# Kernel optimization log

Hardware: AMD Instinct MI355X
Metric: run time of the kernel (lower is better)

The kernel has to match this reference:

```python
import jax, jax.numpy as jnp
import numpy as np

N = 100000   # nodes
E = 1600000  # edges
D = 128      # feature dim (layers all 128)
G = 512      # graphs in batch
C = 10       # num_classes
EPS = 1e-5   # batchnorm eps


def setup_inputs() -> dict:
    key = jax.random.key(0)
    ks = jax.random.split(key, 16)
    s = 1.0 / np.sqrt(D)
    return {
        "x": jax.random.normal(ks[0], (N, D), jnp.float32),
        "edge_index": jax.random.randint(ks[1], (2, E), 0, N),
        "batch": jnp.sort(jax.random.randint(ks[2], (N,), 0, G)),
        "w1": jax.random.normal(ks[3], (D, D), jnp.float32) * s,
        "b1": jnp.zeros((D,), jnp.float32),
        "w2": jax.random.normal(ks[4], (D, D), jnp.float32) * s,
        "b2": jnp.zeros((D,), jnp.float32),
        "w3": jax.random.normal(ks[5], (D, D), jnp.float32) * s,
        "b3": jnp.zeros((D,), jnp.float32),
        "g1": jnp.ones((D,), jnp.float32),
        "be1": jnp.zeros((D,), jnp.float32),
        "g2": jnp.ones((D,), jnp.float32),
        "be2": jnp.zeros((D,), jnp.float32),
        "fc_w": jax.random.normal(ks[6], (D, C), jnp.float32) * s,
        "fc_b": jnp.zeros((C,), jnp.float32),
    }


def _gcn(x, src, dst, norm, W, b):
    # transform -> gather -> normalize -> scatter-add (PyG GCNConv)
    h = x @ W
    out = jax.ops.segment_sum(h[src] * norm[:, None], dst, num_segments=x.shape[0])
    return out + b


def _bn(x, g, b):
    # training-mode BatchNorm1d: batch mean / biased variance
    mu = jnp.mean(x, axis=0)
    var = jnp.mean((x - mu) ** 2, axis=0)
    return (x - mu) * jax.lax.rsqrt(var + EPS) * g + b


def reference(x, edge_index, batch, w1, b1, w2, b2, w3, b3, g1, be1, g2, be2, fc_w, fc_b):
    n = x.shape[0]
    loop = jnp.arange(n)
    src = jnp.concatenate([edge_index[0], loop])  # add self-loops
    dst = jnp.concatenate([edge_index[1], loop])
    deg = jax.ops.segment_sum(jnp.ones_like(src, x.dtype), dst, num_segments=n)
    dinv = jax.lax.rsqrt(jnp.maximum(deg, 1.0))  # deg >= 1 due to self-loops
    norm = dinv[src] * dinv[dst]  # symmetric normalization per edge

    h = jax.nn.relu(_gcn(x, src, dst, norm, w1, b1))        # conv1 + relu (bn1 unused, per source)
    h = jax.nn.relu(_gcn(h, src, dst, norm, w2, b2))        # conv2 + relu
    h = jax.nn.relu(_bn(h, g1, be1))                        # bn + relu
    h = jax.nn.relu(_gcn(h, src, dst, norm, w3, b3))        # conv3 + relu
    h = jax.nn.relu(_bn(h, g2, be2))                        # bn + relu

    cnt = jax.ops.segment_sum(jnp.ones((n,), h.dtype), batch, num_segments=G)
    pooled = jax.ops.segment_sum(h, batch, num_segments=G) / jnp.maximum(cnt, 1.0)[:, None]
    logits = pooled @ fc_w + fc_b
    return jax.nn.log_softmax(logits, axis=1)
```

## Files before the change

kernel.cpp:

```cpp
#include <hip/hip_runtime.h>
#include <hip/hip_bf16.h>
#include <math.h>

#define D 128
#define G_GRAPHS 512
#define C_CLASSES 10
#define BN_EPS 1e-5f
#define NBUCK_MAX 512
#define EDGE_CHUNK 4096
#define EPT 16

typedef unsigned short u16;
typedef unsigned int u32;
typedef unsigned short ushort4_t __attribute__((ext_vector_type(4)));
typedef unsigned short ushort8_t __attribute__((ext_vector_type(8)));
typedef __bf16 bf16x8 __attribute__((ext_vector_type(8)));
typedef float floatx4 __attribute__((ext_vector_type(4)));
union B8 { ushort8_t u; bf16x8 b; };

__device__ __forceinline__ float bf_lo(u32 v) { return __uint_as_float(v << 16); }
__device__ __forceinline__ float bf_hi(u32 v) { return __uint_as_float(v & 0xffff0000u); }
__device__ __forceinline__ u16 f2bf(float f) {
    union { float f; u32 u; } x; x.f = f;
    u32 r = x.u + 0x7fff + ((x.u >> 16) & 1);
    return (u16)(r >> 16);
}
__device__ __forceinline__ u32 pack2bf(float a, float b) {
    return (u32)f2bf(a) | ((u32)f2bf(b) << 16);
}


__global__ __launch_bounds__(256) void bucket_hist_kernel(
    const int* __restrict__ dst, int* __restrict__ bucketCnt, int E, int nbuck)
{
    __shared__ int h[NBUCK_MAX];
    int tid = threadIdx.x;
    for (int i = tid; i < NBUCK_MAX; i += 256) h[i] = 0;
    __syncthreads();
    for (int i = blockIdx.x * 256 + tid; i < E; i += gridDim.x * 256)
        atomicAdd(&h[dst[i] >> 8], 1);
    __syncthreads();
    for (int i = tid; i < nbuck; i += 256)
        if (h[i]) atomicAdd(&bucketCnt[i], h[i]);
}

__global__ void scan_buckets_kernel(
    const int* __restrict__ bucketCnt, int* __restrict__ bucketBase,
    int* __restrict__ bucketCursor, int* __restrict__ rowPtr, int nbuck, int N, int E)
{
    __shared__ int buf[2][512];
    int tid = threadIdx.x;
    int v = (tid < nbuck) ? bucketCnt[tid] : 0;
    buf[0][tid] = v;
    __syncthreads();
    int cur = 0;
    for (int off = 1; off < 512; off <<= 1) {
        buf[1 - cur][tid] = buf[cur][tid] + ((tid >= off) ? buf[cur][tid - off] : 0);
        cur ^= 1;
        __syncthreads();
    }
    if (tid < nbuck) {
        int b = buf[cur][tid] - v;
        bucketBase[tid] = b;
        bucketCursor[tid] = b;
    }
    if (tid == 0) { bucketBase[nbuck] = E; rowPtr[N] = E; }
}

__global__ __launch_bounds__(256) void scatter_pairs_kernel(
    const int* __restrict__ src, const int* __restrict__ dst,
    int* __restrict__ bucketCursor, u32* __restrict__ pairs, int E)
{
    __shared__ int h[NBUCK_MAX];
    __shared__ int base[NBUCK_MAX];
    int tid = threadIdx.x;
    int e0 = blockIdx.x * EDGE_CHUNK;
    for (int i = tid; i < NBUCK_MAX; i += 256) h[i] = 0;
    __syncthreads();
    int s[EPT], d[EPT], r[EPT];
#pragma unroll
    for (int j = 0; j < EPT; ++j) {
        int i = e0 + j * 256 + tid;
        if (i < E) {
            s[j] = src[i];
            d[j] = dst[i];
            r[j] = atomicAdd(&h[d[j] >> 8], 1);
        } else {
            d[j] = -1;
        }
    }
    __syncthreads();
    for (int i = tid; i < NBUCK_MAX; i += 256)
        if (h[i]) base[i] = atomicAdd(&bucketCursor[i], h[i]);
    __syncthreads();
#pragma unroll
    for (int j = 0; j < EPT; ++j) {
        if (d[j] >= 0) {
            int b = d[j] >> 8;
            pairs[base[b] + r[j]] = ((u32)s[j] << 8) | (u32)(d[j] & 255);
        }
    }
}

__global__ __launch_bounds__(256) void bucket_sort_kernel(
    const u32* __restrict__ pairs, const int* __restrict__ bucketBase,
    int* __restrict__ colIdx, int* __restrict__ rowPtr, float* __restrict__ dinv, int N)
{
    __shared__ int h[256];
    __shared__ int cur[256];
    __shared__ int sbuf[2][256];
    int tid = threadIdx.x;
    int b = blockIdx.x;
    int s = bucketBase[b], e = bucketBase[b + 1];
    h[tid] = 0;
    __syncthreads();
    for (int i = s + tid; i < e; i += 256)
        atomicAdd(&h[pairs[i] & 255], 1);
    __syncthreads();
    int cnt = h[tid];
    sbuf[0][tid] = cnt;
    __syncthreads();
    int c = 0;
    for (int off = 1; off < 256; off <<= 1) {
        sbuf[1 - c][tid] = sbuf[c][tid] + ((tid >= off) ? sbuf[c][tid - off] : 0);
        c ^= 1;
        __syncthreads();
    }
    int excl = sbuf[c][tid] - cnt;
    int v = b * 256 + tid;
    if (v < N) {
        rowPtr[v] = s + excl;
        dinv[v] = rsqrtf((float)(cnt + 1));
    }
    cur[tid] = s + excl;
    __syncthreads();
    for (int i = s + tid; i < e; i += 256) {
        u32 p = pairs[i];
        int pos = atomicAdd(&cur[p & 255], 1);
        colIdx[pos] = (int)(p >> 8);
    }
}

__global__ __launch_bounds__(256) void graph_bounds_kernel(
    const int* __restrict__ batch, int* __restrict__ gstart, int N)
{
    int i = blockIdx.x * 256 + threadIdx.x;
    if (i >= N) return;
    int b = batch[i];
    int prev = (i == 0) ? -1 : batch[i - 1];
    if (b != prev) {
        for (int g = prev + 1; g <= b; ++g) gstart[g] = i;
    }
    if (i == N - 1) {
        for (int g = b + 1; g <= G_GRAPHS; ++g) gstart[g] = N;
    }
}

__global__ __launch_bounds__(256) void wconv_kernel(
    const float4* __restrict__ w1, const float4* __restrict__ w2,
    const float4* __restrict__ w3, u16* __restrict__ wtAll)
{
    const float4* W = (blockIdx.x == 0) ? w1 : (blockIdx.x == 1) ? w2 : w3;
    u16* Wt = wtAll + (size_t)blockIdx.x * D * D;
    int tid = threadIdx.x;
#pragma unroll
    for (int i = 0; i < 16; ++i) {
        int idx = tid + i * 256;
        int k = idx >> 5, c4 = idx & 31;
        float4 v = W[idx];
        Wt[(4 * c4 + 0) * D + k] = f2bf(v.x);
        Wt[(4 * c4 + 1) * D + k] = f2bf(v.y);
        Wt[(4 * c4 + 2) * D + k] = f2bf(v.z);
        Wt[(4 * c4 + 3) * D + k] = f2bf(v.w);
    }
}

#define XS_STRIDE 136
#define GEMM_GRID 768

__device__ __forceinline__ void gemm_core_and_store(
    const u16* Xs, const u16* Ws, u16* __restrict__ Y, int row0, int nrows, int tid)
{
    int wid = tid >> 6, lane = tid & 63;
    int m = lane & 15, quad = lane >> 4;
    int xrow = wid * 16 + m;

    floatx4 acc[8] = {};
#pragma unroll
    for (int ks = 0; ks < 4; ++ks) {
        int kk = ks * 32 + quad * 8;
        B8 a;
        a.u = *(const ushort8_t*)&Xs[xrow * XS_STRIDE + kk];
#pragma unroll
        for (int t = 0; t < 8; ++t) {
            B8 b;
            b.u = *(const ushort8_t*)&Ws[(t * 16 + m) * XS_STRIDE + kk];
            acc[t] = __builtin_amdgcn_mfma_f32_16x16x32_bf16(b.b, a.b, acc[t], 0, 0, 0);
        }
    }
    int grow = row0 + xrow;
    if (grow < nrows) {
#pragma unroll
        for (int t = 0; t < 8; ++t) {
            ushort4_t o;
            o.x = f2bf(acc[t][0]); o.y = f2bf(acc[t][1]);
            o.z = f2bf(acc[t][2]); o.w = f2bf(acc[t][3]);
            *(ushort4_t*)&Y[(size_t)grow * D + t * 16 + quad * 4] = o;
        }
    }
}

__device__ __forceinline__ void stage_w(const u16* __restrict__ Wt, u16* Ws, int tid) {
    const ushort8_t* Wv = (const ushort8_t*)Wt;
#pragma unroll
    for (int i = 0; i < 8; ++i) {
        int idx = tid + i * 256;
        int n = idx >> 4, c8 = idx & 15;
        *(ushort8_t*)&Ws[n * XS_STRIDE + c8 * 8] = Wv[idx];
    }
}

__global__ __launch_bounds__(256) void gemm_mfma_f32in_kernel(
    const float4* __restrict__ X, const u16* __restrict__ Wt,
    u16* __restrict__ Y, int nrows, int ntiles)
{
    __shared__ __align__(16) u16 Xs[64 * XS_STRIDE];
    __shared__ __align__(16) u16 Ws[128 * XS_STRIDE];
    int tid = threadIdx.x;
    stage_w(Wt, Ws, tid);
    for (int t = blockIdx.x; t < ntiles; t += gridDim.x) {
        int row0 = t * 64;
        __syncthreads();
#pragma unroll
        for (int i = 0; i < 8; ++i) {
            int idx = tid + i * 256;
            int r = idx >> 5, c4 = idx & 31;
            int gr = row0 + r;
            float4 v = make_float4(0.f, 0.f, 0.f, 0.f);
            if (gr < nrows) v = X[(size_t)gr * 32 + c4];
            ushort4_t o;
            o.x = f2bf(v.x); o.y = f2bf(v.y); o.z = f2bf(v.z); o.w = f2bf(v.w);
            *(ushort4_t*)&Xs[r * XS_STRIDE + c4 * 4] = o;
        }
        __syncthreads();
        gemm_core_and_store(Xs, Ws, Y, row0, nrows, tid);
    }
}

__global__ __launch_bounds__(256) void gemm_mfma_bf16in_kernel(
    const uint4* __restrict__ X, const u16* __restrict__ Wt,
    const float* __restrict__ gsum, const float* __restrict__ gsq,
    const float* __restrict__ gamma, const float* __restrict__ beta, float invN,
    u16* __restrict__ Y, int nrows, int ntiles)
{
    __shared__ __align__(16) u16 Xs[64 * XS_STRIDE];
    __shared__ __align__(16) u16 Ws[128 * XS_STRIDE];
    __shared__ float scs[D], shs[D];
    int tid = threadIdx.x;
    bool fuse = (gsum != nullptr);
    stage_w(Wt, Ws, tid);
    if (fuse && tid < D) {
        float mu = gsum[tid] * invN;
        float var = gsq[tid] * invN - mu * mu;
        float sc = gamma[tid] * rsqrtf(var + BN_EPS);
        scs[tid] = sc;
        shs[tid] = beta[tid] - mu * sc;
    }
    for (int t = blockIdx.x; t < ntiles; t += gridDim.x) {
        int row0 = t * 64;
        __syncthreads();
#pragma unroll
        for (int i = 0; i < 4; ++i) {
            int idx = tid + i * 256;
            int r = idx >> 4, c8 = idx & 15;
            int gr = row0 + r;
            uint4 v = make_uint4(0, 0, 0, 0);
            if (gr < nrows) v = X[(size_t)gr * 16 + c8];
            if (fuse) {
                int k = c8 * 8;
                v.x = pack2bf(fmaxf(bf_lo(v.x) * scs[k]     + shs[k],     0.f),
                              fmaxf(bf_hi(v.x) * scs[k + 1] + shs[k + 1], 0.f));
                v.y = pack2bf(fmaxf(bf_lo(v.y) * scs[k + 2] + shs[k + 2], 0.f),
                              fmaxf(bf_hi(v.y) * scs[k + 3] + shs[k + 3], 0.f));
                v.z = pack2bf(fmaxf(bf_lo(v.z) * scs[k + 4] + shs[k + 4], 0.f),
                              fmaxf(bf_hi(v.z) * scs[k + 5] + shs[k + 5], 0.f));
                v.w = pack2bf(fmaxf(bf_lo(v.w) * scs[k + 6] + shs[k + 6], 0.f),
                              fmaxf(bf_hi(v.w) * scs[k + 7] + shs[k + 7], 0.f));
            }
            *(uint4*)&Xs[r * XS_STRIDE + c8 * 8] = v;
        }
        __syncthreads();
        gemm_core_and_store(Xs, Ws, Y, row0, nrows, tid);
    }
}

#define ACC8(tw, duu)                                              \
    acc[0] += (duu) * bf_lo((tw).x); acc[1] += (duu) * bf_hi((tw).x); \
    acc[2] += (duu) * bf_lo((tw).y); acc[3] += (duu) * bf_hi((tw).y); \
    acc[4] += (duu) * bf_lo((tw).z); acc[5] += (duu) * bf_hi((tw).z); \
    acc[6] += (duu) * bf_lo((tw).w); acc[7] += (duu) * bf_hi((tw).w);

__global__ __launch_bounds__(256) void aggregate_kernel(
    const uint4* __restrict__ T, const int* __restrict__ colIdx,
    const int* __restrict__ rowPtr, const float* __restrict__ dinv,
    const float* __restrict__ bias, uint4* __restrict__ outH, int n)
{
    int wid = threadIdx.x >> 6;
    int lane = threadIdx.x & 63;
    int fg = lane & 15;
    int eg = lane >> 4;
    int row = (blockIdx.x * 4 + wid) * 4 + eg;
    bool active = row < n;

    float dr = 0.f;
    int s = 0, m = 0;
    float acc[8] = {};
    if (active) {
        dr = dinv[row];
        s = rowPtr[row];
        m = rowPtr[row + 1] - s;
        uint4 sv = T[(size_t)row * 16 + fg];
        acc[0] = dr * bf_lo(sv.x); acc[1] = dr * bf_hi(sv.x);
        acc[2] = dr * bf_lo(sv.y); acc[3] = dr * bf_hi(sv.y);
        acc[4] = dr * bf_lo(sv.z); acc[5] = dr * bf_hi(sv.z);
        acc[6] = dr * bf_lo(sv.w); acc[7] = dr * bf_hi(sv.w);
    }

    for (int c0 = 0; c0 < m; c0 += 16) {
        int mm = m - c0;
        if (mm > 16) mm = 16;
        int u = row;
        float du = 0.f;
        if (fg < mm) {
            u = colIdx[s + c0 + fg];
            du = dinv[u];
        }
        int nb = (mm + 3) >> 2;
        for (int b = 0; b < nb; ++b) {
            int base = (eg << 4) + (b << 2);
            int u0 = __shfl(u, base);     float d0 = __shfl(du, base);
            int u1 = __shfl(u, base + 1); float d1 = __shfl(du, base + 1);
            int u2 = __shfl(u, base + 2); float d2 = __shfl(du, base + 2);
            int u3 = __shfl(u, base + 3); float d3 = __shfl(du, base + 3);
            uint4 t0 = T[(size_t)u0 * 16 + fg];
            uint4 t1 = T[(size_t)u1 * 16 + fg];
            uint4 t2 = T[(size_t)u2 * 16 + fg];
            uint4 t3 = T[(size_t)u3 * 16 + fg];
            ACC8(t0, d0); ACC8(t1, d1); ACC8(t2, d2); ACC8(t3, d3);
        }
    }

    if (active) {
        const float4* bp = (const float4*)bias;
        float4 b0 = bp[fg * 2], b1 = bp[fg * 2 + 1];
        uint4 o;
        o.x = pack2bf(fmaxf(dr * acc[0] + b0.x, 0.f), fmaxf(dr * acc[1] + b0.y, 0.f));
        o.y = pack2bf(fmaxf(dr * acc[2] + b0.z, 0.f), fmaxf(dr * acc[3] + b0.w, 0.f));
        o.z = pack2bf(fmaxf(dr * acc[4] + b1.x, 0.f), fmaxf(dr * acc[5] + b1.y, 0.f));
        o.w = pack2bf(fmaxf(dr * acc[6] + b1.z, 0.f), fmaxf(dr * acc[7] + b1.w, 0.f));
        outH[(size_t)row * 16 + fg] = o;
    }
}

__global__ __launch_bounds__(256) void bn_stats_kernel(
    const u32* __restrict__ H, int n, float* __restrict__ gsum, float* __restrict__ gsq)
{
    int tid = threadIdx.x;
    int c = tid & 63, rr = tid >> 6;
    float sA = 0.f, sA2 = 0.f, sB = 0.f, sB2 = 0.f;
    for (int row = blockIdx.x * 4 + rr; row < n; row += gridDim.x * 4) {
        u32 v = H[(size_t)row * 64 + c];
        float a = bf_lo(v), b = bf_hi(v);
        sA += a; sA2 += a * a; sB += b; sB2 += b * b;
    }
    __shared__ float shA[256], shA2[256], shB[256], shB2[256];
    shA[tid] = sA; shA2[tid] = sA2; shB[tid] = sB; shB2[tid] = sB2;
    __syncthreads();
    if (tid < 64) {
        float tA = shA[tid] + shA[tid + 64] + shA[tid + 128] + shA[tid + 192];
        float tA2 = shA2[tid] + shA2[tid + 64] + shA2[tid + 128] + shA2[tid + 192];
        float tB = shB[tid] + shB[tid + 64] + shB[tid + 128] + shB[tid + 192];
        float tB2 = shB2[tid] + shB2[tid + 64] + shB2[tid + 128] + shB2[tid + 192];
        atomicAdd(&gsum[2 * c], tA);
        atomicAdd(&gsq[2 * c], tA2);
        atomicAdd(&gsum[2 * c + 1], tB);
        atomicAdd(&gsq[2 * c + 1], tB2);
    }
}

__global__ __launch_bounds__(256) void pool_classify_kernel(
    const u32* __restrict__ H, const float* __restrict__ gsum, const float* __restrict__ gsq,
    const float* __restrict__ gamma, const float* __restrict__ beta, float invN,
    const int* __restrict__ gstart, const float* __restrict__ fcw,
    const float* __restrict__ fcb, float* __restrict__ out)
{
    int g = blockIdx.x;
    int tid = threadIdx.x;
    int c = tid & 63, q = tid >> 6;
    float muA = gsum[2 * c] * invN, muB = gsum[2 * c + 1] * invN;
    float vA = gsq[2 * c] * invN - muA * muA, vB = gsq[2 * c + 1] * invN - muB * muB;
    float scA = gamma[2 * c] * rsqrtf(vA + BN_EPS), scB = gamma[2 * c + 1] * rsqrtf(vB + BN_EPS);
    float shA = beta[2 * c] - muA * scA, shB = beta[2 * c + 1] - muB * scB;

    int s = gstart[g], cnt = gstart[g + 1] - s;
    float aA = 0.f, aB = 0.f;
    for (int i = q; i < cnt; i += 4) {
        u32 v = H[(size_t)(s + i) * 64 + c];
        aA += fmaxf(bf_lo(v) * scA + shA, 0.f);
        aB += fmaxf(bf_hi(v) * scB + shB, 0.f);
    }
    __shared__ float sA[256], sB[256];
    __shared__ float prow[D];
    __shared__ float lg[C_CLASSES];
    sA[tid] = aA; sB[tid] = aB;
    __syncthreads();
    if (tid < 64) {
        float tA = sA[tid] + sA[tid + 64] + sA[tid + 128] + sA[tid + 192];
        float tB = sB[tid] + sB[tid + 64] + sB[tid + 128] + sB[tid + 192];
        float inv = 1.f / (float)(cnt > 1 ? cnt : 1);
        prow[2 * tid] = tA * inv;
        prow[2 * tid + 1] = tB * inv;
    }
    __syncthreads();
    if (tid < C_CLASSES) {
        float sum = fcb[tid];
        for (int d = 0; d < D; ++d) sum += prow[d] * fcw[d * C_CLASSES + tid];
        lg[tid] = sum;
    }
    __syncthreads();
    if (tid == 0) {
        float mx = -1e30f;
        for (int k = 0; k < C_CLASSES; ++k) mx = fmaxf(mx, lg[k]);
        float se = 0.f;
        for (int k = 0; k < C_CLASSES; ++k) se += expf(lg[k] - mx);
        float lse = mx + logf(se);
        for (int k = 0; k < C_CLASSES; ++k) out[(size_t)g * C_CLASSES + k] = lg[k] - lse;
    }
}

extern "C" void kernel_launch(void* const* d_in, const int* in_sizes, int n_in,
                              void* d_out, int out_size, void* d_ws, size_t ws_size,
                              hipStream_t stream) {
    const float* x   = (const float*)d_in[0];
    const int* ei    = (const int*)d_in[1];
    const int* batch = (const int*)d_in[2];
    const float* w1  = (const float*)d_in[3];
    const float* b1  = (const float*)d_in[4];
    const float* w2  = (const float*)d_in[5];
    const float* b2  = (const float*)d_in[6];
    const float* w3  = (const float*)d_in[7];
    const float* b3  = (const float*)d_in[8];
    const float* g1  = (const float*)d_in[9];
    const float* be1 = (const float*)d_in[10];
    const float* g2  = (const float*)d_in[11];
    const float* be2 = (const float*)d_in[12];
    const float* fcw = (const float*)d_in[13];
    const float* fcb = (const float*)d_in[14];

    const int N = in_sizes[0] / D;
    const int E = in_sizes[1] / 2;
    const int* src = ei;
    const int* dst = ei + E;
    const int nbuck = (N + 255) >> 8;
    const float invN = 1.f / (float)N;

    char* p = (char*)d_ws;
    auto alloc = [&](size_t bytes) -> void* {
        void* r = (void*)p;
        p += (bytes + 255) & ~(size_t)255;
        return r;
    };
    int*   bucketCnt    = (int*)alloc(NBUCK_MAX * 4);
    float* statsacc     = (float*)alloc(4 * D * 4);
    float* gsum1 = statsacc, *gsq1 = statsacc + D, *gsum2 = statsacc + 2 * D, *gsq2 = statsacc + 3 * D;
    float* dinv     = (float*)alloc((size_t)N * 4);
    int*   rowPtr   = (int*)alloc((size_t)(N + 1) * 4);
    int*   colIdx   = (int*)alloc((size_t)E * 4);
    u32*   pairs    = (u32*)alloc((size_t)E * 4);
    int*   bucketBase   = (int*)alloc((NBUCK_MAX + 1) * 4);
    int*   bucketCursor = (int*)alloc(NBUCK_MAX * 4);
    int*   gstart  = (int*)alloc((G_GRAPHS + 1) * 4);
    u16*   wtAll   = (u16*)alloc((size_t)3 * D * D * 2);
    u16*   tmp     = (u16*)alloc((size_t)N * D * 2);
    u16*   hbuf    = (u16*)alloc((size_t)N * D * 2);

    hipMemsetAsync(bucketCnt, 0, NBUCK_MAX * 4 + 4 * D * 4, stream);

    bucket_hist_kernel<<<512, 256, 0, stream>>>(dst, bucketCnt, E, nbuck);
    scan_buckets_kernel<<<1, 512, 0, stream>>>(bucketCnt, bucketBase, bucketCursor, rowPtr, nbuck, N, E);
    scatter_pairs_kernel<<<(E + EDGE_CHUNK - 1) / EDGE_CHUNK, 256, 0, stream>>>(src, dst, bucketCursor, pairs, E);
    bucket_sort_kernel<<<nbuck, 256, 0, stream>>>(pairs, bucketBase, colIdx, rowPtr, dinv, N);
    graph_bounds_kernel<<<(N + 255) / 256, 256, 0, stream>>>(batch, gstart, N);
    wconv_kernel<<<3, 256, 0, stream>>>((const float4*)w1, (const float4*)w2, (const float4*)w3, wtAll);

    const int NT = (N + 63) / 64;
    const int GB = NT < GEMM_GRID ? NT : GEMM_GRID;
    const int AB = (N + 15) / 16;

    gemm_mfma_f32in_kernel<<<GB, 256, 0, stream>>>((const float4*)x, wtAll, tmp, N, NT);
    aggregate_kernel<<<AB, 256, 0, stream>>>((const uint4*)tmp, colIdx, rowPtr, dinv, b1, (uint4*)hbuf, N);
    gemm_mfma_bf16in_kernel<<<GB, 256, 0, stream>>>((const uint4*)hbuf, wtAll + D * D,
        nullptr, nullptr, nullptr, nullptr, 0.f, tmp, N, NT);
    aggregate_kernel<<<AB, 256, 0, stream>>>((const uint4*)tmp, colIdx, rowPtr, dinv, b2, (uint4*)hbuf, N);
    bn_stats_kernel<<<256, 256, 0, stream>>>((const u32*)hbuf, N, gsum1, gsq1);
    gemm_mfma_bf16in_kernel<<<GB, 256, 0, stream>>>((const uint4*)hbuf, wtAll + 2 * D * D,
        gsum1, gsq1, g1, be1, invN, tmp, N, NT);
    aggregate_kernel<<<AB, 256, 0, stream>>>((const uint4*)tmp, colIdx, rowPtr, dinv, b3, (uint4*)hbuf, N);
    bn_stats_kernel<<<256, 256, 0, stream>>>((const u32*)hbuf, N, gsum2, gsq2);
    pool_classify_kernel<<<G_GRAPHS, 256, 0, stream>>>((const u32*)hbuf, gsum2, gsq2, g2, be2, invN,
        gstart, fcw, fcb, (float*)d_out);
}
```

Before: 515.2 us.

## Fuse BatchNorm statistics into aggregation and make aggregate kernel grid-stride

The aggregate kernel now loops over row tiles in a grid-stride fashion, with each block handling about four tiles. It can also accumulate per-feature sum and sum-of-squares of its ReLU outputs and reduce them through shared-memory then global atomics. This removes the two standalone bn_stats passes that re-read the full hidden buffer. The GEMM grid is also changed from a fixed cap to half the tile count. The cost is extra registers and atomics in the aggregation, and statistics now come from pre-rounding float values instead of the stored bf16 values.

```diff
diff --git a/kernel.cpp b/kernel.cpp
--- a/kernel.cpp
+++ b/kernel.cpp
@@ -176,7 +176,6 @@
 }
 
 #define XS_STRIDE 136
-#define GEMM_GRID 768
 
 __device__ __forceinline__ void gemm_core_and_store(
     const u16* Xs, const u16* Ws, u16* __restrict__ Y, int row0, int nrows, int tid)
@@ -303,88 +302,102 @@
 __global__ __launch_bounds__(256) void aggregate_kernel(
     const uint4* __restrict__ T, const int* __restrict__ colIdx,
     const int* __restrict__ rowPtr, const float* __restrict__ dinv,
-    const float* __restrict__ bias, uint4* __restrict__ outH, int n)
-{
-    int wid = threadIdx.x >> 6;
-    int lane = threadIdx.x & 63;
+    const float* __restrict__ bias, uint4* __restrict__ outH, int n, int ntiles,
+    float* __restrict__ gsum, float* __restrict__ gsq)
+{
+    int tid = threadIdx.x;
+    int wid = tid >> 6;
+    int lane = tid & 63;
     int fg = lane & 15;
     int eg = lane >> 4;
-    int row = (blockIdx.x * 4 + wid) * 4 + eg;
-    bool active = row < n;
-
-    float dr = 0.f;
-    int s = 0, m = 0;
-    float acc[8] = {};
-    if (active) {
-        dr = dinv[row];
-        s = rowPtr[row];
-        m = rowPtr[row + 1] - s;
-        uint4 sv = T[(size_t)row * 16 + fg];
-        acc[0] = dr * bf_lo(sv.x); acc[1] = dr * bf_hi(sv.x);
-        acc[2] = dr * bf_lo(sv.y); acc[3] = dr * bf_hi(sv.y);
-        acc[4] = dr * bf_lo(sv.z); acc[5] = dr * bf_hi(sv.z);
-        acc[6] = dr * bf_lo(sv.w); acc[7] = dr * bf_hi(sv.w);
-    }
-
-    for (int c0 = 0; c0 < m; c0 += 16) {
-        int mm = m - c0;
-        if (mm > 16) mm = 16;
-        int u = row;
-        float du = 0.f;
-        if (fg < mm) {
-            u = colIdx[s + c0 + fg];
-            du = dinv[u];
-        }
-        int nb = (mm + 3) >> 2;
-        for (int b = 0; b < nb; ++b) {
-            int base = (eg << 4) + (b << 2);
-            int u0 = __shfl(u, base);     float d0 = __shfl(du, base);
-            int u1 = __shfl(u, base + 1); float d1 = __shfl(du, base + 1);
-            int u2 = __shfl(u, base + 2); float d2 = __shfl(du, base + 2);
-            int u3 = __shfl(u, base + 3); float d3 = __shfl(du, base + 3);
-            uint4 t0 = T[(size_t)u0 * 16 + fg];
-            uint4 t1 = T[(size_t)u1 * 16 + fg];
-            uint4 t2 = T[(size_t)u2 * 16 + fg];
-            uint4 t3 = T[(size_t)u3 * 16 + fg];
-            ACC8(t0, d0); ACC8(t1, d1); ACC8(t2, d2); ACC8(t3, d3);
-        }
-    }
-
-    if (active) {
-        const float4* bp = (const float4*)bias;
-        float4 b0 = bp[fg * 2], b1 = bp[fg * 2 + 1];
-        uint4 o;
-        o.x = pack2bf(fmaxf(dr * acc[0] + b0.x, 0.f), fmaxf(dr * acc[1] + b0.y, 0.f));
-        o.y = pack2bf(fmaxf(dr * acc[2] + b0.z, 0.f), fmaxf(dr * acc[3] + b0.w, 0.f));
-        o.z = pack2bf(fmaxf(dr * acc[4] + b1.x, 0.f), fmaxf(dr * acc[5] + b1.y, 0.f));
-        o.w = pack2bf(fmaxf(dr * acc[6] + b1.z, 0.f), fmaxf(dr * acc[7] + b1.w, 0.f));
-        outH[(size_t)row * 16 + fg] = o;
-    }
-}
-
-__global__ __launch_bounds__(256) void bn_stats_kernel(
-    const u32* __restrict__ H, int n, float* __restrict__ gsum, float* __restrict__ gsq)
-{
-    int tid = threadIdx.x;
-    int c = tid & 63, rr = tid >> 6;
-    float sA = 0.f, sA2 = 0.f, sB = 0.f, sB2 = 0.f;
-    for (int row = blockIdx.x * 4 + rr; row < n; row += gridDim.x * 4) {
-        u32 v = H[(size_t)row * 64 + c];
-        float a = bf_lo(v), b = bf_hi(v);
-        sA += a; sA2 += a * a; sB += b; sB2 += b * b;
-    }
-    __shared__ float shA[256], shA2[256], shB[256], shB2[256];
-    shA[tid] = sA; shA2[tid] = sA2; shB[tid] = sB; shB2[tid] = sB2;
-    __syncthreads();
-    if (tid < 64) {
-        float tA = shA[tid] + shA[tid + 64] + shA[tid + 128] + shA[tid + 192];
-        float tA2 = shA2[tid] + shA2[tid + 64] + shA2[tid + 128] + shA2[tid + 192];
-        float tB = shB[tid] + shB[tid + 64] + shB[tid + 128] + shB[tid + 192];
-        float tB2 = shB2[tid] + shB2[tid + 64] + shB2[tid + 128] + shB2[tid + 192];
-        atomicAdd(&gsum[2 * c], tA);
-        atomicAdd(&gsq[2 * c], tA2);
-        atomicAdd(&gsum[2 * c + 1], tB);
-        atomicAdd(&gsq[2 * c + 1], tB2);
+    bool doStats = (gsum != nullptr);
+    float ssum[8] = {}, ssq[8] = {};
+
+    const float4* bp = (const float4*)bias;
+    float4 b0 = bp[fg * 2], b1 = bp[fg * 2 + 1];
+
+    for (int tile = blockIdx.x; tile < ntiles; tile += gridDim.x) {
+        int row = (tile * 4 + wid) * 4 + eg;
+        bool active = row < n;
+
+        float dr = 0.f;
+        int s = 0, m = 0;
+        float acc[8] = {};
+        if (active) {
+            dr = dinv[row];
+            s = rowPtr[row];
+            m = rowPtr[row + 1] - s;
+            uint4 sv = T[(size_t)row * 16 + fg];
+            acc[0] = dr * bf_lo(sv.x); acc[1] = dr * bf_hi(sv.x);
+            acc[2] = dr * bf_lo(sv.y); acc[3] = dr * bf_hi(sv.y);
+            acc[4] = dr * bf_lo(sv.z); acc[5] = dr * bf_hi(sv.z);
+            acc[6] = dr * bf_lo(sv.w); acc[7] = dr * bf_hi(sv.w);
+        }
+
+        for (int c0 = 0; c0 < m; c0 += 16) {
+            int mm = m - c0;
+            if (mm > 16) mm = 16;
+            int u = row;
+            float du = 0.f;
+            if (fg < mm) {
+                u = colIdx[s + c0 + fg];
+                du = dinv[u];
+            }
+            int nb = (mm + 3) >> 2;
+            for (int b = 0; b < nb; ++b) {
+                int base = (eg << 4) + (b << 2);
+                int u0 = __shfl(u, base);     float d0 = __shfl(du, base);
+                int u1 = __shfl(u, base + 1); float d1 = __shfl(du, base + 1);
+                int u2 = __shfl(u, base + 2); float d2 = __shfl(du, base + 2);
+                int u3 = __shfl(u, base + 3); float d3 = __shfl(du, base + 3);
+                uint4 t0 = T[(size_t)u0 * 16 + fg];
+                uint4 t1 = T[(size_t)u1 * 16 + fg];
+                uint4 t2 = T[(size_t)u2 * 16 + fg];
+                uint4 t3 = T[(size_t)u3 * 16 + fg];
+                ACC8(t0, d0); ACC8(t1, d1); ACC8(t2, d2); ACC8(t3, d3);
+            }
+        }
+
+        if (active) {
+            float hv[8];
+            hv[0] = fmaxf(dr * acc[0] + b0.x, 0.f);
+            hv[1] = fmaxf(dr * acc[1] + b0.y, 0.f);
+            hv[2] = fmaxf(dr * acc[2] + b0.z, 0.f);
+            hv[3] = fmaxf(dr * acc[3] + b0.w, 0.f);
+            hv[4] = fmaxf(dr * acc[4] + b1.x, 0.f);
+            hv[5] = fmaxf(dr * acc[5] + b1.y, 0.f);
+            hv[6] = fmaxf(dr * acc[6] + b1.z, 0.f);
+            hv[7] = fmaxf(dr * acc[7] + b1.w, 0.f);
+            uint4 o;
+            o.x = pack2bf(hv[0], hv[1]);
+            o.y = pack2bf(hv[2], hv[3]);
+            o.z = pack2bf(hv[4], hv[5]);
+            o.w = pack2bf(hv[6], hv[7]);
+            outH[(size_t)row * 16 + fg] = o;
+            if (doStats) {
+#pragma unroll
+                for (int j = 0; j < 8; ++j) {
+                    ssum[j] += hv[j];
+                    ssq[j] += hv[j] * hv[j];
+                }
+            }
+        }
+    }
+
+    if (doStats) {
+        __shared__ float lsum[D], lsq[D];
+        if (tid < D) { lsum[tid] = 0.f; lsq[tid] = 0.f; }
+        __syncthreads();
+#pragma unroll
+        for (int j = 0; j < 8; ++j) {
+            atomicAdd(&lsum[fg * 8 + j], ssum[j]);
+            atomicAdd(&lsq[fg * 8 + j], ssq[j]);
+        }
+        __syncthreads();
+        if (tid < D) {
+            atomicAdd(&gsum[tid], lsum[tid]);
+            atomicAdd(&gsq[tid], lsq[tid]);
+        }
     }
 }
 
@@ -494,19 +507,21 @@
     wconv_kernel<<<3, 256, 0, stream>>>((const float4*)w1, (const float4*)w2, (const float4*)w3, wtAll);
 
     const int NT = (N + 63) / 64;
-    const int GB = NT < GEMM_GRID ? NT : GEMM_GRID;
-    const int AB = (N + 15) / 16;
+    const int GB = (NT + 1) / 2;
+    const int AT = (N + 15) / 16;
+    const int AGB = (AT + 3) / 4;
 
     gemm_mfma_f32in_kernel<<<GB, 256, 0, stream>>>((const float4*)x, wtAll, tmp, N, NT);
-    aggregate_kernel<<<AB, 256, 0, stream>>>((const uint4*)tmp, colIdx, rowPtr, dinv, b1, (uint4*)hbuf, N);
+    aggregate_kernel<<<AGB, 256, 0, stream>>>((const uint4*)tmp, colIdx, rowPtr, dinv, b1,
+        (uint4*)hbuf, N, AT, nullptr, nullptr);
     gemm_mfma_bf16in_kernel<<<GB, 256, 0, stream>>>((const uint4*)hbuf, wtAll + D * D,
         nullptr, nullptr, nullptr, nullptr, 0.f, tmp, N, NT);
-    aggregate_kernel<<<AB, 256, 0, stream>>>((const uint4*)tmp, colIdx, rowPtr, dinv, b2, (uint4*)hbuf, N);
-    bn_stats_kernel<<<256, 256, 0, stream>>>((const u32*)hbuf, N, gsum1, gsq1);
+    aggregate_kernel<<<AGB, 256, 0, stream>>>((const uint4*)tmp, colIdx, rowPtr, dinv, b2,
+        (uint4*)hbuf, N, AT, gsum1, gsq1);
     gemm_mfma_bf16in_kernel<<<GB, 256, 0, stream>>>((const uint4*)hbuf, wtAll + 2 * D * D,
         gsum1, gsq1, g1, be1, invN, tmp, N, NT);
-    aggregate_kernel<<<AB, 256, 0, stream>>>((const uint4*)tmp, colIdx, rowPtr, dinv, b3, (uint4*)hbuf, N);
-    bn_stats_kernel<<<256, 256, 0, stream>>>((const u32*)hbuf, N, gsum2, gsq2);
+    aggregate_kernel<<<AGB, 256, 0, stream>>>((const uint4*)tmp, colIdx, rowPtr, dinv, b3,
+        (uint4*)hbuf, N, AT, gsum2, gsq2);
     pool_classify_kernel<<<G_GRAPHS, 256, 0, stream>>>((const u32*)hbuf, gsum2, gsq2, g2, be2, invN,
         gstart, fcw, fcb, (float*)d_out);
 }
```

Result: slower. 528.1 us (+2.5%).
